# Kernel tuning notes

Measured on AMD Instinct MI355X. Metric: run time of the kernel, lower is better.

The kernel has to match this reference:

```python
import jax, jax.numpy as jnp
import numpy as np

B, S, D, H = 4, 4096, 1024, 1024  # batch, seq, token_dim (d+1), hidden_dim
WIN, STRIDE, GLOB = 256, 128, 16
EPS = 1e-5
SCALE = 1.0 / np.sqrt(H).astype(np.float32)


def build_sparse_causal_mask(seq_len):
    i = jnp.arange(seq_len)[:, None]
    j = jnp.arange(seq_len)[None, :]
    causal = j <= i
    allowed = causal & ((i - j) < WIN)          # local window
    allowed = allowed | (((i - j) % STRIDE == 0) & causal)  # strided
    allowed = allowed | ((j < GLOB) & causal)   # global tokens
    return allowed  # [S, S] bool


def layer_norm(x, g, b):
    m = jnp.mean(x, axis=-1, keepdims=True)
    v = jnp.mean(jnp.square(x - m), axis=-1, keepdims=True)
    return (x - m) * jax.lax.rsqrt(v + EPS) * g + b


def setup_inputs() -> dict:
    key = jax.random.key(0)
    ks = jax.random.split(key, 5)
    gain = 0.01
    # xavier_uniform bound for square [H,D] matrices
    def xavier(k, shape):
        bound = gain * np.sqrt(6.0 / (shape[0] + shape[1]))
        return jax.random.uniform(k, shape, jnp.float32, -bound, bound)
    return {
        "tokens": jax.random.normal(ks[0], (B, S, D), jnp.float32),
        "Wq": xavier(ks[1], (D, H)),
        "Wk": xavier(ks[2], (D, H)),
        "Wv": xavier(ks[3], (D, D)),
        "Wo": xavier(ks[4], (D, D)),
        "g1": jnp.ones((D,), jnp.float32),
        "b1": jnp.zeros((D,), jnp.float32),
        "g2": jnp.ones((D,), jnp.float32),
        "b2": jnp.zeros((D,), jnp.float32),
    }


def reference(tokens, Wq, Wk, Wv, Wo, g1, b1, g2, b2):
    x = layer_norm(tokens, g1, b1)                    # [B,S,D]
    Q = jnp.einsum("bsd,dh->bsh", x, Wq)              # [B,S,H]
    K = jnp.einsum("bsd,dh->bsh", x, Wk)
    V = jnp.einsum("bsd,de->bse", x, Wv)              # [B,S,D]
    scores = jnp.einsum("bqh,bkh->bqk", Q, K) * SCALE  # [B,S,S]
    allowed = build_sparse_causal_mask(S)
    scores = jnp.where(allowed, scores, -jnp.inf)
    weights = jax.nn.softmax(scores, axis=-1)
    attn = jnp.einsum("bqk,bkd->bqd", weights, V)     # [B,S,D]
    out = tokens + jnp.einsum("bsd,de->bse", attn, Wo) * 0.1
    return layer_norm(out, g2, b2)
```

## Files before the change

kernel.cpp:

```cpp
#include <hip/hip_runtime.h>

#define S_LEN   4096
#define D_DIM   1024
#define WIN_    256
#define STRIDE_ 128
#define GLOB_   16
#define SCALE_F 0.03125f
#define EPS_F   1e-5f

typedef __bf16 bf16x8 __attribute__((ext_vector_type(8)));
typedef float  f32x4  __attribute__((ext_vector_type(4)));

__device__ __forceinline__ float b2f(unsigned short u) {
    union { unsigned int i; float f; } c; c.i = ((unsigned int)u) << 16; return c.f;
}
__device__ __forceinline__ unsigned short f2bf(float f) {
    union { float f; unsigned int i; } c; c.f = f;
    unsigned int u = c.i;
    u += 0x7fffu + ((u >> 16) & 1u);
    return (unsigned short)(u >> 16);
}

__device__ __forceinline__ void gld_lds16(const void* g, void* l) {
    __builtin_amdgcn_global_load_lds(
        (const __attribute__((address_space(1))) unsigned int*)g,
        (__attribute__((address_space(3))) unsigned int*)l, 16, 0, 0);
}

__device__ __forceinline__ float blk_sum(float v, float* red, int tid) {
    int lane = tid & 63, wv = tid >> 6;
    #pragma unroll
    for (int m = 32; m >= 1; m >>= 1) v += __shfl_xor(v, m, 64);
    __syncthreads();
    if (lane == 0) red[wv] = v;
    __syncthreads();
    return red[0] + red[1] + red[2] + red[3];
}

__global__ __launch_bounds__(256) void ln_full_kernel(
    const float* __restrict__ in, float* __restrict__ mu, float* __restrict__ rs,
    const float* __restrict__ g, const float* __restrict__ bb,
    unsigned short* __restrict__ xb) {
    __shared__ float red[4];
    int row = blockIdx.x, tid = threadIdx.x;
    size_t off = (size_t)row * D_DIM + tid * 4;
    float4 r = *(const float4*)(in + off);
    float s = blk_sum(r.x + r.y + r.z + r.w, red, tid);
    float mean = s * (1.0f / 1024.0f);
    float d0 = r.x - mean, d1 = r.y - mean, d2 = r.z - mean, d3 = r.w - mean;
    float s2 = blk_sum(d0*d0 + d1*d1 + d2*d2 + d3*d3, red, tid);
    float rstd = rsqrtf(s2 * (1.0f / 1024.0f) + EPS_F);
    if (tid == 0) { mu[row] = mean; rs[row] = rstd; }
    float4 gr = *(const float4*)(g  + tid * 4);
    float4 br = *(const float4*)(bb + tid * 4);
    ushort4 o;
    o.x = f2bf(d0 * rstd * gr.x + br.x);
    o.y = f2bf(d1 * rstd * gr.y + br.y);
    o.z = f2bf(d2 * rstd * gr.z + br.z);
    o.w = f2bf(d3 * rstd * gr.w + br.w);
    *(ushort4*)(xb + off) = o;
}

__global__ __launch_bounds__(256) void ln2_inplace_kernel(
    float* __restrict__ data, const float* __restrict__ g,
    const float* __restrict__ bb) {
    __shared__ float red[4];
    int row = blockIdx.x, tid = threadIdx.x;
    size_t off = (size_t)row * D_DIM + tid * 4;
    float4 v = *(const float4*)(data + off);
    float s = blk_sum(v.x + v.y + v.z + v.w, red, tid);
    float mean = s * (1.0f / 1024.0f);
    float d0 = v.x - mean, d1 = v.y - mean, d2 = v.z - mean, d3 = v.w - mean;
    float s2 = blk_sum(d0*d0 + d1*d1 + d2*d2 + d3*d3, red, tid);
    float rstd = rsqrtf(s2 * (1.0f / 1024.0f) + EPS_F);
    float4 gr = *(const float4*)(g  + tid * 4);
    float4 br = *(const float4*)(bb + tid * 4);
    float4 o;
    o.x = d0 * rstd * gr.x + br.x;
    o.y = d1 * rstd * gr.y + br.y;
    o.z = d2 * rstd * gr.z + br.z;
    o.w = d3 * rstd * gr.w + br.w;
    *(float4*)(data + off) = o;
}

__global__ __launch_bounds__(256) void transpose_cvt(
    const float* __restrict__ in, unsigned short* __restrict__ outp) {
    __shared__ unsigned short tile[32][33];
    int tid = threadIdx.x;
    int tx = tid & 31, ty = tid >> 5;
    int bx = blockIdx.x * 32, by = blockIdx.y * 32;
    #pragma unroll
    for (int r = 0; r < 32; r += 8)
        tile[ty + r][tx] = f2bf(in[(size_t)(by + ty + r) * 1024 + bx + tx]);
    __syncthreads();
    #pragma unroll
    for (int r = 0; r < 32; r += 8)
        outp[(size_t)(bx + ty + r) * 1024 + by + tx] = tile[tx][ty + r];
}

__global__ __launch_bounds__(256) void transpose1024(
    const unsigned short* __restrict__ in, unsigned short* __restrict__ outp) {
    __shared__ unsigned short tile[32][33];
    int tid = threadIdx.x;
    int tx = tid & 31, ty = tid >> 5;
    int bx = blockIdx.x * 32, by = blockIdx.y * 32;
    #pragma unroll
    for (int r = 0; r < 32; r += 8)
        tile[ty + r][tx] = in[(size_t)(by + ty + r) * 1024 + bx + tx];
    __syncthreads();
    #pragma unroll
    for (int r = 0; r < 32; r += 8)
        outp[(size_t)(bx + ty + r) * 1024 + by + tx] = tile[tx][ty + r];
}

__global__ __launch_bounds__(256) void transln_kernel(
    const float* __restrict__ tok, const float* __restrict__ mu,
    const float* __restrict__ rs, const float* __restrict__ g,
    const float* __restrict__ bb, unsigned short* __restrict__ xbT) {
    __shared__ unsigned short tile[32][33];
    int tid = threadIdx.x;
    int tx = tid & 31, ty = tid >> 5;
    int s0 = blockIdx.x * 32;
    int n0 = blockIdx.y * 32;
    int b  = blockIdx.z;
    float gv = g[n0 + tx], bv = bb[n0 + tx];
    #pragma unroll
    for (int r = 0; r < 32; r += 8) {
        int grow = (b << 12) + s0 + ty + r;
        float v = tok[(size_t)grow * 1024 + n0 + tx];
        tile[ty + r][tx] = f2bf((v - mu[grow]) * rs[grow] * gv + bv);
    }
    __syncthreads();
    #pragma unroll
    for (int r = 0; r < 32; r += 8)
        xbT[((size_t)b * 1024 + n0 + ty + r) * 4096 + s0 + tx] = tile[tx][ty + r];
}

__global__ __launch_bounds__(256) void gemm_small(
    const float* __restrict__ A32, const float* __restrict__ W32,
    unsigned short* __restrict__ C16) {
    const int K = 1024, N = 1024;
    __shared__ __align__(16) unsigned short As[64][40];
    __shared__ __align__(16) unsigned short Bs[64][40];
    int tid  = threadIdx.x;
    int lane = tid & 63, wv = tid >> 6;
    int lm   = lane & 15, quad = lane >> 4;
    int m0 = blockIdx.y * 64, n0 = blockIdx.x * 64;
    int srow = tid >> 2, scg = tid & 3;
    int bk   = tid >> 3, bn  = (tid & 7) * 8;

    f32x4 acc[4] = {};
    for (int k0 = 0; k0 < K; k0 += 32) {
        const float* ap = A32 + (size_t)(m0 + srow) * K + k0 + scg * 8;
        float4 p = *(const float4*)(ap);
        float4 q = *(const float4*)(ap + 4);
        union { uint4 u; unsigned short s[8]; } w;
        w.s[0]=f2bf(p.x); w.s[1]=f2bf(p.y); w.s[2]=f2bf(p.z); w.s[3]=f2bf(p.w);
        w.s[4]=f2bf(q.x); w.s[5]=f2bf(q.y); w.s[6]=f2bf(q.z); w.s[7]=f2bf(q.w);
        *(uint4*)&As[srow][scg * 8] = w.u;

        const float* wp = W32 + (size_t)(k0 + bk) * N + n0 + bn;
        float4 a = *(const float4*)wp, b = *(const float4*)(wp + 4);
        float wvv[8] = {a.x,a.y,a.z,a.w,b.x,b.y,b.z,b.w};
        #pragma unroll
        for (int e = 0; e < 8; ++e) Bs[bn + e][bk] = f2bf(wvv[e]);
        __syncthreads();
        bf16x8 af = *(const bf16x8*)&As[wv * 16 + lm][quad * 8];
        #pragma unroll
        for (int t = 0; t < 4; ++t) {
            bf16x8 bfr = *(const bf16x8*)&Bs[t * 16 + lm][quad * 8];
            acc[t] = __builtin_amdgcn_mfma_f32_16x16x32_bf16(af, bfr, acc[t], 0, 0, 0);
        }
        __syncthreads();
    }
    #pragma unroll
    for (int t = 0; t < 4; ++t) {
        int col = n0 + t * 16 + lm;
        #pragma unroll
        for (int r = 0; r < 4; ++r) {
            int row = m0 + wv * 16 + quad * 4 + r;
            C16[(size_t)row * N + col] = f2bf(acc[t][r]);
        }
    }
}

template <bool EPI>
__global__ __launch_bounds__(256) void gemm128(
    const unsigned short* __restrict__ A, const unsigned short* __restrict__ BT,
    unsigned short* __restrict__ C16, float* __restrict__ Cres,
    const float* __restrict__ tok) {
    const int K = 1024, N = 1024;
    __shared__ __align__(16) unsigned short As[4096];
    __shared__ __align__(16) unsigned short Bs[4096];
    int tid = threadIdx.x, lane = tid & 63, wv = tid >> 6;
    int lm = lane & 15, quad = lane >> 4;
    int wr = wv >> 1, wc = wv & 1;
    int flat = blockIdx.y * 8 + blockIdx.x;
    int logical = ((flat & 7) << 7) | (flat >> 3);
    int m0 = (logical >> 3) * 128, n0 = (logical & 7) * 128;

    f32x4 acc[4][4] = {};

    const unsigned short* ga0 = A  + (size_t)(m0 + lane) * K + wv * 8;
    const unsigned short* ga1 = A  + (size_t)(m0 + 64 + lane) * K + wv * 8;
    const unsigned short* gb0 = BT + (size_t)(n0 + lane) * K + wv * 8;
    const unsigned short* gb1 = BT + (size_t)(n0 + 64 + lane) * K + wv * 8;
    unsigned short* la0 = &As[wv * 1024 + lane * 8];
    unsigned short* la1 = &As[wv * 1024 + 512 + lane * 8];
    unsigned short* lb0 = &Bs[wv * 1024 + lane * 8];
    unsigned short* lb1 = &Bs[wv * 1024 + 512 + lane * 8];

    for (int k0 = 0; k0 < K; k0 += 32) {
        gld_lds16(ga0 + k0, la0);
        gld_lds16(ga1 + k0, la1);
        gld_lds16(gb0 + k0, lb0);
        gld_lds16(gb1 + k0, lb1);
        __syncthreads();
        bf16x8 af[4], bfr[4];
        #pragma unroll
        for (int t = 0; t < 4; ++t) {
            af[t]  = *(const bf16x8*)&As[quad * 1024 + (wr * 64 + t * 16 + lm) * 8];
            bfr[t] = *(const bf16x8*)&Bs[quad * 1024 + (wc * 64 + t * 16 + lm) * 8];
        }
        #pragma unroll
        for (int mt = 0; mt < 4; ++mt)
            #pragma unroll
            for (int nt = 0; nt < 4; ++nt)
                acc[mt][nt] = __builtin_amdgcn_mfma_f32_16x16x32_bf16(
                    af[mt], bfr[nt], acc[mt][nt], 0, 0, 0);
        __syncthreads();
    }
    #pragma unroll
    for (int mt = 0; mt < 4; ++mt) {
        #pragma unroll
        for (int nt = 0; nt < 4; ++nt) {
            int col = n0 + wc * 64 + nt * 16 + lm;
            #pragma unroll
            for (int r = 0; r < 4; ++r) {
                int row = m0 + wr * 64 + mt * 16 + quad * 4 + r;
                size_t idx = (size_t)row * N + col;
                if (EPI) Cres[idx] = tok[idx] + 0.1f * acc[mt][nt][r];
                else     C16[idx]  = f2bf(acc[mt][nt][r]);
            }
        }
    }
}

#define NT_MAX 48
#define SCROW  776
__global__ __launch_bounds__(256) void attn16_kernel(
    const unsigned short* __restrict__ Q, const unsigned short* __restrict__ K,
    const unsigned short* __restrict__ XT, unsigned short* __restrict__ Ao) {
    __shared__ __align__(16) unsigned short Ps[16 * SCROW];
    int tid = threadIdx.x, lane = tid & 63, wv = tid >> 6;
    int lm = lane & 15, quad = lane >> 4;
    int bxr = blockIdx.x;
    int xcd = bxr & 7;
    int sl  = bxr >> 3;
    int batch = xcd >> 1;
    int ptyp  = xcd & 1;
    int t = ptyp ? (64 + sl)
                 : ((sl < 64) ? sl : (128 + sl));
    int bx = batch * 256 + t;
    int b  = bx >> 8;
    int i0 = (bx & 255) << 4;
    int rowbase = (b << 12) + i0;
    int wlo = i0 - 256; if (wlo < 0) wlo = 0;
    int nwin = ((i0 - wlo) >> 4) + 1;
    int tmax = (i0 - 16) / 128;
    int nstr = tmax - 2; if (nstr < 0) nstr = 0;
    int nglob = (wlo > 0) ? 1 : 0;
    int ntiles = nwin + nstr + nglob;
    int ntp = (ntiles + 3) & ~3;

    const unsigned short* Qg = Q + (size_t)(rowbase + lm) * 1024 + quad * 8;

    const unsigned short* Kbp = K + (((size_t)b << 12) << 10);
    for (int tg = wv * 4; tg < ntp; tg += 16) {
        f32x4 acc[4] = {};
        int tb[4];
        #pragma unroll
        for (int c = 0; c < 4; ++c) {
            int t = tg + c, base = 0;
            if (t < nwin) base = wlo + (t << 4);
            else if (t - nwin < nstr) base = i0 - 128 * (3 + (t - nwin));
            tb[c] = base;
        }
        for (int k0 = 0; k0 < 1024; k0 += 32) {
            bf16x8 a = *(const bf16x8*)(Qg + k0);
            #pragma unroll
            for (int c = 0; c < 4; ++c) {
                bf16x8 bb = *(const bf16x8*)(Kbp +
                    (size_t)(tb[c] + lm) * 1024 + k0 + quad * 8);
                acc[c] = __builtin_amdgcn_mfma_f32_16x16x32_bf16(a, bb, acc[c], 0, 0, 0);
            }
        }
        #pragma unroll
        for (int c = 0; c < 4; ++c) {
            int t = tg + c;
            int j = tb[c] + lm;
            bool pad = (t >= ntiles);
            #pragma unroll
            for (int r = 0; r < 4; ++r) {
                int i = i0 + quad * 4 + r;
                int diff = i - j;
                bool ok = !pad && (j <= i) &&
                          (diff < 256 || (diff & 127) == 0 || j < 16);
                Ps[(quad * 4 + r) * SCROW + (t << 4) + lm] =
                    f2bf(ok ? acc[c][r] : -1e30f);
            }
        }
    }
    __syncthreads();

    int ncol = ntp << 4;
    for (int q = wv * 4; q < wv * 4 + 4; ++q) {
        unsigned short* row = &Ps[q * SCROW];
        float mx = -1e30f;
        for (int c = lane; c < ncol; c += 64) mx = fmaxf(mx, b2f(row[c]));
        #pragma unroll
        for (int m = 32; m >= 1; m >>= 1) mx = fmaxf(mx, __shfl_xor(mx, m, 64));
        float sm = 0.f;
        for (int c = lane; c < ncol; c += 64)
            sm += __expf(SCALE_F * (b2f(row[c]) - mx));
        #pragma unroll
        for (int m = 32; m >= 1; m >>= 1) sm += __shfl_xor(sm, m, 64);
        float inv = 1.0f / sm;
        for (int c = lane; c < ncol; c += 64)
            row[c] = f2bf(__expf(SCALE_F * (b2f(row[c]) - mx)) * inv);
    }
    __syncthreads();

    int n0w = wv * 256;
    const unsigned short* Xb = XT + ((size_t)b << 10) * 4096;
    f32x4 oacc[16] = {};
    int nch = ntp >> 1;
    for (int c = 0; c < nch; ++c) {
        int t0 = 2 * c, t1 = 2 * c + 1;
        int b0 = (t0 < nwin) ? wlo + (t0 << 4)
               : ((t0 - nwin < nstr) ? i0 - 128 * (3 + t0 - nwin) : 0);
        int b1 = (t1 < nwin) ? wlo + (t1 << 4)
               : ((t1 - nwin < nstr) ? i0 - 128 * (3 + t1 - nwin) : 0);
        bf16x8 a = *(const bf16x8*)&Ps[lm * SCROW + (c << 5) + quad * 8];
        int kb = (quad < 2) ? (b0 + quad * 8) : (b1 + (quad - 2) * 8);
        const unsigned short* xp = Xb + kb;
        #pragma unroll
        for (int nt = 0; nt < 16; ++nt) {
            bf16x8 bb = *(const bf16x8*)(xp + (size_t)(n0w + nt * 16 + lm) * 4096);
            oacc[nt] = __builtin_amdgcn_mfma_f32_16x16x32_bf16(a, bb, oacc[nt], 0, 0, 0);
        }
    }
    #pragma unroll
    for (int nt = 0; nt < 16; ++nt) {
        int col = n0w + nt * 16 + lm;
        #pragma unroll
        for (int r = 0; r < 4; ++r) {
            int row = rowbase + quad * 4 + r;
            Ao[(size_t)row * 1024 + col] = f2bf(oacc[nt][r]);
        }
    }
}

extern "C" void kernel_launch(void* const* d_in, const int* in_sizes, int n_in,
                              void* d_out, int out_size, void* d_ws, size_t ws_size,
                              hipStream_t stream) {
    const float* tokens = (const float*)d_in[0];
    const float* Wq = (const float*)d_in[1];
    const float* Wk = (const float*)d_in[2];
    const float* Wv = (const float*)d_in[3];
    const float* Wo = (const float*)d_in[4];
    const float* g1 = (const float*)d_in[5];
    const float* b1 = (const float*)d_in[6];
    const float* g2 = (const float*)d_in[7];
    const float* b2 = (const float*)d_in[8];
    float* out = (float*)d_out;
    char* ws = (char*)d_ws;

    const size_t MB = 1048576;
    float* mu = (float*)(ws);
    float* rs = (float*)(ws + 65536);
    unsigned short* WqT    = (unsigned short*)(ws + 1 * MB);
    unsigned short* WkT    = (unsigned short*)(ws + 3 * MB);
    unsigned short* Wfused = (unsigned short*)(ws + 5 * MB);
    unsigned short* WfT    = (unsigned short*)(ws + 7 * MB);
    unsigned short* Qb     = (unsigned short*)(ws + 9 * MB);
    unsigned short* xb     = (unsigned short*)d_out;
    unsigned short* xbT    = (unsigned short*)d_out;
    unsigned short* Kb     = (unsigned short*)d_out + 16777216;
    unsigned short* attnX  = Qb;

    dim3 b256(256);
    const int ROWS = 4 * S_LEN;
    dim3 tg(32, 32);
    dim3 gsmall(16, 16);
    dim3 g128(8, 128);
    dim3 gtl(128, 32, 4);

    ln_full_kernel<<<ROWS, b256, 0, stream>>>(tokens, mu, rs, g1, b1, xb);
    transpose_cvt<<<tg, b256, 0, stream>>>(Wq, WqT);
    transpose_cvt<<<tg, b256, 0, stream>>>(Wk, WkT);
    gemm_small<<<gsmall, b256, 0, stream>>>(Wv, Wo, Wfused);
    transpose1024<<<tg, b256, 0, stream>>>(Wfused, WfT);
    gemm128<false><<<g128, b256, 0, stream>>>(xb, WqT, Qb, nullptr, nullptr);
    gemm128<false><<<g128, b256, 0, stream>>>(xb, WkT, Kb, nullptr, nullptr);
    transln_kernel<<<gtl, b256, 0, stream>>>(tokens, mu, rs, g1, b1, xbT);
    attn16_kernel<<<1024, b256, 0, stream>>>(Qb, Kb, xbT, attnX);
    gemm128<true><<<g128, b256, 0, stream>>>(attnX, WfT, nullptr, out, tokens);
    ln2_inplace_kernel<<<ROWS, b256, 0, stream>>>(out, g2, b2);
}
```

Measured before the change: 720.5 us.

## Store normalized activations in 16x16 tiled layout for attention PV loads

```diff
diff --git a/kernel.cpp b/kernel.cpp
--- a/kernel.cpp
+++ b/kernel.cpp
@@ -113,11 +113,11 @@
         outp[(size_t)(bx + ty + r) * 1024 + by + tx] = tile[tx][ty + r];
 }
 
-__global__ __launch_bounds__(256) void transln_kernel(
+__global__ __launch_bounds__(256) void transln16_kernel(
     const float* __restrict__ tok, const float* __restrict__ mu,
     const float* __restrict__ rs, const float* __restrict__ g,
-    const float* __restrict__ bb, unsigned short* __restrict__ xbT) {
-    __shared__ unsigned short tile[32][33];
+    const float* __restrict__ bb, unsigned short* __restrict__ X16) {
+    __shared__ unsigned short Lt[32][36];
     int tid = threadIdx.x;
     int tx = tid & 31, ty = tid >> 5;
     int s0 = blockIdx.x * 32;
@@ -128,12 +128,18 @@
     for (int r = 0; r < 32; r += 8) {
         int grow = (b << 12) + s0 + ty + r;
         float v = tok[(size_t)grow * 1024 + n0 + tx];
-        tile[ty + r][tx] = f2bf((v - mu[grow]) * rs[grow] * gv + bv);
-    }
-    __syncthreads();
-    #pragma unroll
-    for (int r = 0; r < 32; r += 8)
-        xbT[((size_t)b * 1024 + n0 + ty + r) * 4096 + s0 + tx] = tile[tx][ty + r];
+        Lt[tx][ty + r] = f2bf((v - mu[grow]) * rs[grow] * gv + bv);
+    }
+    __syncthreads();
+    int tt  = tid >> 6;
+    int sTl = tt >> 1, nTl = tt & 1;
+    int idx = tid & 63;
+    int nl  = idx >> 2, so4 = (idx & 3) << 2;
+    uint2 v = *(const uint2*)&Lt[nTl * 16 + nl][sTl * 16 + so4];
+    size_t off = (size_t)b * 4194304 +
+        (((size_t)(((s0 >> 4) + sTl) * 64 + (n0 >> 4) + nTl)) << 8) +
+        (nl << 4) + so4;
+    *(uint2*)(X16 + off) = v;
 }
 
 __global__ __launch_bounds__(256) void gemm_small(
@@ -332,7 +338,9 @@
     __syncthreads();
 
     int n0w = wv * 256;
-    const unsigned short* Xb = XT + ((size_t)b << 10) * 4096;
+    int nT0 = wv << 4;
+    const unsigned short* Xb = XT + (size_t)b * 4194304;
+    int octet = quad & 1, tsel = quad >> 1;
     f32x4 oacc[16] = {};
     int nch = ntp >> 1;
     for (int c = 0; c < nch; ++c) {
@@ -342,12 +350,13 @@
         int b1 = (t1 < nwin) ? wlo + (t1 << 4)
                : ((t1 - nwin < nstr) ? i0 - 128 * (3 + t1 - nwin) : 0);
         bf16x8 a = *(const bf16x8*)&Ps[lm * SCROW + (c << 5) + quad * 8];
-        int kb = (quad < 2) ? (b0 + quad * 8) : (b1 + (quad - 2) * 8);
-        const unsigned short* xp = Xb + kb;
+        int sT = (tsel ? b1 : b0) >> 4;
+        const unsigned short* xp = Xb + (((size_t)(sT * 64 + nT0)) << 8)
+                                      + (lm << 4) + (octet << 3);
         #pragma unroll
         for (int nt = 0; nt < 16; ++nt) {
-            bf16x8 bb = *(const bf16x8*)(xp + (size_t)(n0w + nt * 16 + lm) * 4096);
-            oacc[nt] = __builtin_amdgcn_mfma_f32_16x16x32_bf16(a, bb, oacc[nt], 0, 0, 0);
+            bf16x8 bb2 = *(const bf16x8*)(xp + (nt << 8));
+            oacc[nt] = __builtin_amdgcn_mfma_f32_16x16x32_bf16(a, bb2, oacc[nt], 0, 0, 0);
         }
     }
     #pragma unroll
@@ -385,7 +394,7 @@
     unsigned short* WfT    = (unsigned short*)(ws + 7 * MB);
     unsigned short* Qb     = (unsigned short*)(ws + 9 * MB);
     unsigned short* xb     = (unsigned short*)d_out;
-    unsigned short* xbT    = (unsigned short*)d_out;
+    unsigned short* X16    = (unsigned short*)d_out;
     unsigned short* Kb     = (unsigned short*)d_out + 16777216;
     unsigned short* attnX  = Qb;
 
@@ -403,8 +412,8 @@
     transpose1024<<<tg, b256, 0, stream>>>(Wfused, WfT);
     gemm128<false><<<g128, b256, 0, stream>>>(xb, WqT, Qb, nullptr, nullptr);
     gemm128<false><<<g128, b256, 0, stream>>>(xb, WkT, Kb, nullptr, nullptr);
-    transln_kernel<<<gtl, b256, 0, stream>>>(tokens, mu, rs, g1, b1, xbT);
-    attn16_kernel<<<1024, b256, 0, stream>>>(Qb, Kb, xbT, attnX);
+    transln16_kernel<<<gtl, b256, 0, stream>>>(tokens, mu, rs, g1, b1, X16);
+    attn16_kernel<<<1024, b256, 0, stream>>>(Qb, Kb, X16, attnX);
     gemm128<true><<<g128, b256, 0, stream>>>(attnX, WfT, nullptr, out, tokens);
     ln2_inplace_kernel<<<ROWS, b256, 0, stream>>>(out, g2, b2);
 }
```

Result: faster. 668.1 us (-7.3%).
